# Performance work log

Hardware: AMD Instinct MI355X
Metric: run time of the kernel (lower is better)

## Reference

```python
import jax, jax.numpy as jnp
import numpy as np


def _sincos_1d(dim, L):
    # standard 1D sin-cos embedding: (L, dim), dim even
    half = dim // 2
    omega = 1.0 / (10000.0 ** (jnp.arange(half, dtype=jnp.float32) / half))  # (half,)
    out = jnp.arange(L, dtype=jnp.float32)[:, None] * omega[None, :]         # (L, half)
    return jnp.concatenate([jnp.sin(out), jnp.cos(out)], axis=1)            # (L, dim)


def setup_inputs() -> dict:
    key = jax.random.key(0)
    k1, k2, k3, k4 = jax.random.split(key, 4)
    B, C, T, H, W = 4, 2, 8, 128, 128
    D, P = 512, 32
    y_obs = jax.random.normal(k1, (B, C, T, H, W), dtype=jnp.float32)
    mask1 = jax.random.randint(k2, (B, 1, T, H, W), 0, 2).astype(jnp.int32)
    y_obs = y_obs * mask1.astype(jnp.float32)  # unobserved voxels are 0
    proj_w = jax.random.normal(k3, (D, C + 3 * P), dtype=jnp.float32) * 0.05
    proj_b = jax.random.normal(k4, (D,), dtype=jnp.float32) * 0.05
    return {"y_obs": y_obs, "mask1": mask1, "proj_w": proj_w, "proj_b": proj_b, "M_max": 65536}


def reference(y_obs, mask1, proj_w, proj_b, M_max):
    B, C, T, H, W = y_obs.shape
    N = T * H * W
    P = (proj_w.shape[1] - C) // 3  # pos_dim_each
    et = _sincos_1d(P, T)  # (T, P)
    eh = _sincos_1d(P, H)  # (H, P)
    ew = _sincos_1d(P, W)  # (W, P)

    # stream-compact nonzero voxel positions (row-major order = torch nonzero order)
    mflat = (mask1[:, 0].reshape(B, N) != 0)                       # (B, N)
    pos = jnp.where(mflat, jnp.arange(N, dtype=jnp.int32)[None, :], N)
    spos = jnp.sort(pos, axis=1)[:, :M_max]                        # (B, M)
    valid = spos < N                                               # (B, M)
    idx = jnp.minimum(spos, N - 1)                                 # safe gather index

    t_idx = idx // (H * W)
    h_idx = (idx // W) % H
    w_idx = idx % W

    # gather observed values: (B, M, C)
    vals = jnp.take_along_axis(y_obs.reshape(B, C, N), idx[:, None, :], axis=2)
    vals = jnp.transpose(vals, (0, 2, 1))

    feat = jnp.concatenate([vals, et[t_idx], eh[h_idx], ew[w_idx]], axis=-1)  # (B, M, C+3P)
    feat = jnp.where(valid[..., None], feat, 0.0)  # padded rows are zero features (torch pads zeros)

    cond_tokens = jnp.einsum('bmf,df->bmd', feat, proj_w) + proj_b  # (B, M, D)
    pad_mask = ~valid                                               # True == padding
    return cond_tokens, pad_mask
```

## Files before the change

### kernel.cpp

```cpp
#include <hip/hip_runtime.h>
#include <stdint.h>

#define BB    4
#define CC    2
#define TT    8
#define HH    128
#define WW    128
#define NN    131072
#define DD    512
#define PP    32
#define FF    98
#define KP    104
#define MMAX  65536

#define WT_OFF   0
#define CIDX_OFF 212992
#define TAB_OFF  (CIDX_OFF + 1048576)
#define CNT_OFF  (TAB_OFF + 33792)
#define OFFS_OFF (CNT_OFF + 8192)
#define TOT_OFF  (OFFS_OFF + 8192)

__global__ void k_prep(const float* __restrict__ w, float* __restrict__ tab,
                       float* __restrict__ wt) {
    int i = blockIdx.x * 256 + threadIdx.x;
    if (i < 8448) {
        int pos, j;
        if (i < 256)            { pos = i >> 5;            j = i & 31; }
        else if (i < 256+4096)  { int ii = i - 256;        pos = ii >> 5; j = ii & 31; }
        else                    { int ii = i - 256 - 4096; pos = ii >> 5; j = ii & 31; }
        int jj = (j < 16) ? j : (j - 16);
        float omega = 1.0f / powf(10000.0f, (float)jj * (1.0f/16.0f));
        float arg = (float)pos * omega;
        tab[i] = (j < 16) ? sinf(arg) : cosf(arg);
    }
    int k = i - 8448;
    if (k >= 0 && k < KP * DD) {
        int f = k >> 9, d = k & 511;
        wt[k] = (f < FF) ? w[d * FF + f] : 0.0f;
    }
}

__global__ void k_count(const int* __restrict__ mask, int* __restrict__ cnt) {
    int b = blockIdx.y;
    int i = blockIdx.x * 256 + threadIdx.x;
    int m = (mask[b * NN + i] != 0);
    uint64_t bal = __ballot(m);
    __shared__ int wc[4];
    int lane = threadIdx.x & 63, wv = threadIdx.x >> 6;
    if (lane == 0) wc[wv] = __popcll(bal);
    __syncthreads();
    if (threadIdx.x == 0) cnt[b * 512 + blockIdx.x] = wc[0] + wc[1] + wc[2] + wc[3];
}

__global__ void k_scan(const int* __restrict__ cnt, int* __restrict__ offs, int* __restrict__ tot) {
    int b = blockIdx.x, t = threadIdx.x;
    __shared__ int s[512];
    int v0 = cnt[b * 512 + t];
    s[t] = v0;
    __syncthreads();
    for (int off = 1; off < 512; off <<= 1) {
        int add = (t >= off) ? s[t - off] : 0;
        __syncthreads();
        s[t] += add;
        __syncthreads();
    }
    offs[b * 512 + t] = s[t] - v0;
    if (t == 511) tot[b] = s[511];
}

__global__ void k_scatter(const int* __restrict__ mask, const int* __restrict__ offs,
                          int* __restrict__ cidx) {
    int b = blockIdx.y;
    int i = blockIdx.x * 256 + threadIdx.x;
    int m = (mask[b * NN + i] != 0);
    uint64_t bal = __ballot(m);
    int lane = threadIdx.x & 63, wv = threadIdx.x >> 6;
    __shared__ int wc[4];
    if (lane == 0) wc[wv] = __popcll(bal);
    __syncthreads();
    int woff = 0;
    for (int k = 0; k < wv; ++k) woff += wc[k];
    int rank = __popcll(bal & ((1ull << lane) - 1ull));
    if (m) {
        int r = offs[b * 512 + blockIdx.x] + woff + rank;
        if (r < MMAX) cidx[b * MMAX + r] = i;
    }
}

__global__ __launch_bounds__(256) void k_gemm(
    const float* __restrict__ yobs, const int* __restrict__ cidx,
    const float* __restrict__ tab,  const float* __restrict__ wt,
    const float* __restrict__ bias, const int* __restrict__ tot,
    float* __restrict__ out, float* __restrict__ pm)
{
    __shared__ float As[KP][64];
    __shared__ float Bs[KP][64];
    int bid = blockIdx.x;
    int mt = bid & 1023;
    int b  = bid >> 10;
    int m0 = mt << 6;
    int tid = threadIdx.x;
    int totb = tot[b];

    if (tid < 64)
        pm[(b << 16) + m0 + tid] = ((m0 + tid) >= totb) ? 1.0f : 0.0f;

    {
        int m = tid & 63, q = tid >> 6;
        bool val = (m0 + m) < totb;
        int idx = 0, tt = 0, hh = 0, ww = 0;
        if (val) {
            idx = cidx[(b << 16) + m0 + m];
            tt = idx >> 14; hh = (idx >> 7) & 127; ww = idx & 127;
        }
        const float* et = tab;
        const float* eh = tab + 256;
        const float* ew = tab + 4352;
        for (int k = q; k < KP; k += 4) {
            float f = 0.0f;
            if (val) {
                if (k < 2)       f = yobs[((b * 2 + k) << 17) + idx];
                else if (k < 34) f = et[(tt << 5) + k - 2];
                else if (k < 66) f = eh[(hh << 5) + k - 34];
                else if (k < 98) f = ew[(ww << 5) + k - 66];
            }
            As[k][m] = f;
        }
    }

    int tx = tid & 15, ty = tid >> 4;
    const float4* ap = (const float4*)As + ty;
    const float4* bp = (const float4*)Bs + tx;

    for (int dt = 0; dt < 8; ++dt) {
        for (int i = tid; i < KP * 16; i += 256) {
            int f = i >> 4, d4 = i & 15;
            *(float4*)&Bs[f][d4 << 2] = *(const float4*)&wt[(f << 9) + (dt << 6) + (d4 << 2)];
        }
        __syncthreads();

        float acc[4][4] = {};
        #pragma unroll 4
        for (int k = 0; k < KP; ++k) {
            float4 a  = ap[k * 16];
            float4 w4 = bp[k * 16];
            float av[4] = {a.x, a.y, a.z, a.w};
            float wv[4] = {w4.x, w4.y, w4.z, w4.w};
            #pragma unroll
            for (int i = 0; i < 4; ++i)
                #pragma unroll
                for (int j = 0; j < 4; ++j)
                    acc[i][j] = fmaf(av[i], wv[j], acc[i][j]);
        }

        float4 b4 = *(const float4*)&bias[(dt << 6) + (tx << 2)];
        float bv[4] = {b4.x, b4.y, b4.z, b4.w};
        size_t row0 = ((size_t)((b << 16) + m0 + (ty << 2))) * DD + (dt << 6) + (tx << 2);
        #pragma unroll
        for (int i = 0; i < 4; ++i) {
            float4 r;
            r.x = acc[i][0] + bv[0];
            r.y = acc[i][1] + bv[1];
            r.z = acc[i][2] + bv[2];
            r.w = acc[i][3] + bv[3];
            *(float4*)&out[row0 + (size_t)i * DD] = r;
        }
        __syncthreads();
    }
}

extern "C" void kernel_launch(void* const* d_in, const int* in_sizes, int n_in,
                              void* d_out, int out_size, void* d_ws, size_t ws_size,
                              hipStream_t stream) {
    const float* yobs  = (const float*)d_in[0];
    const int*   mask  = (const int*)d_in[1];
    const float* projw = (const float*)d_in[2];
    const float* projb = (const float*)d_in[3];

    char* ws = (char*)d_ws;
    float* wt   = (float*)(ws + WT_OFF);
    int*   cidx = (int*)  (ws + CIDX_OFF);
    float* tab  = (float*)(ws + TAB_OFF);
    int*   cnt  = (int*)  (ws + CNT_OFF);
    int*   offs = (int*)  (ws + OFFS_OFF);
    int*   tot  = (int*)  (ws + TOT_OFF);

    float* cond = (float*)d_out;
    float* pm   = (float*)d_out + (size_t)BB * MMAX * DD;

    k_prep<<<(8448 + KP * DD + 255) / 256, 256, 0, stream>>>(projw, tab, wt);
    k_count<<<dim3(512, BB), 256, 0, stream>>>(mask, cnt);
    k_scan<<<BB, 512, 0, stream>>>(cnt, offs, tot);
    k_scatter<<<dim3(512, BB), 256, 0, stream>>>(mask, offs, cidx);
    k_gemm<<<BB * 1024, 256, 0, stream>>>(yobs, cidx, tab, wt, projb, tot, cond, pm);
}
```

Baseline: 797.2 us.

## Use split-bf16 MFMA for projection GEMM with swizzled LDS feature tile

Replaces the scalar fp32 FMA GEMM with bf16 MFMA 32x32x16 instructions. The fp32 accuracy is approximated by splitting each operand into high and low bf16 parts and summing three cross products. Weights are pre-split and laid out K-major in the prep kernel, with K padded to 128 and the channel values moved to the end. Features are gathered per row with float4 table loads into an XOR-swizzled LDS tile, and B fragments now come straight from global memory with no LDS staging. The aim is to cut ALU time so the kernel is limited by output bandwidth, at the cost of a slightly lower-precision result than true fp32.

```diff
diff --git a/kernel.cpp b/kernel.cpp
--- a/kernel.cpp
+++ b/kernel.cpp
@@ -3,25 +3,36 @@
 
 #define BB    4
 #define CC    2
-#define TT    8
-#define HH    128
-#define WW    128
 #define NN    131072
 #define DD    512
-#define PP    32
 #define FF    98
-#define KP    104
+#define K2    128
 #define MMAX  65536
 
-#define WT_OFF   0
-#define CIDX_OFF 212992
-#define TAB_OFF  (CIDX_OFF + 1048576)
-#define CNT_OFF  (TAB_OFF + 33792)
-#define OFFS_OFF (CNT_OFF + 8192)
-#define TOT_OFF  (OFFS_OFF + 8192)
+
+#define BTH_OFF  0
+#define BTL_OFF  131072
+#define TAB_OFF  262144
+#define CIDX_OFF 295936
+#define CNT_OFF  1344512
+#define OFFS_OFF 1352704
+#define TOT_OFF  1360896
+
+typedef short  s16x8  __attribute__((ext_vector_type(8)));
+typedef float  f32x16 __attribute__((ext_vector_type(16)));
+
+__device__ __forceinline__ unsigned short f2bf(float x) {
+    uint32_t u = __builtin_bit_cast(uint32_t, x);
+    u += 0x7fffu + ((u >> 16) & 1u);
+    return (unsigned short)(u >> 16);
+}
+__device__ __forceinline__ float bf2f(unsigned short h) {
+    uint32_t u = ((uint32_t)h) << 16;
+    return __builtin_bit_cast(float, u);
+}
 
 __global__ void k_prep(const float* __restrict__ w, float* __restrict__ tab,
-                       float* __restrict__ wt) {
+                       unsigned short* __restrict__ bth, unsigned short* __restrict__ btl) {
     int i = blockIdx.x * 256 + threadIdx.x;
     if (i < 8448) {
         int pos, j;
@@ -34,9 +45,14 @@
         tab[i] = (j < 16) ? sinf(arg) : cosf(arg);
     }
     int k = i - 8448;
-    if (k >= 0 && k < KP * DD) {
-        int f = k >> 9, d = k & 511;
-        wt[k] = (f < FF) ? w[d * FF + f] : 0.0f;
+    if (k >= 0 && k < DD * K2) {
+        int d = k >> 7, kk = k & 127;
+        float v = 0.0f;
+        if (kk < 96)      v = w[d * FF + kk + 2];
+        else if (kk < 98) v = w[d * FF + (kk - 96)];
+        unsigned short h = f2bf(v);
+        bth[k] = h;
+        btl[k] = f2bf(v - bf2f(h));
     }
 }
 
@@ -89,12 +105,12 @@
 
 __global__ __launch_bounds__(256) void k_gemm(
     const float* __restrict__ yobs, const int* __restrict__ cidx,
-    const float* __restrict__ tab,  const float* __restrict__ wt,
+    const float* __restrict__ tab,
+    const unsigned short* __restrict__ bth, const unsigned short* __restrict__ btl,
     const float* __restrict__ bias, const int* __restrict__ tot,
     float* __restrict__ out, float* __restrict__ pm)
 {
-    __shared__ float As[KP][64];
-    __shared__ float Bs[KP][64];
+    __shared__ unsigned short As[2][64 * 128];
     int bid = blockIdx.x;
     int mt = bid & 1023;
     int b  = bid >> 10;
@@ -106,66 +122,89 @@
         pm[(b << 16) + m0 + tid] = ((m0 + tid) >= totb) ? 1.0f : 0.0f;
 
     {
-        int m = tid & 63, q = tid >> 6;
-        bool val = (m0 + m) < totb;
-        int idx = 0, tt = 0, hh = 0, ww = 0;
+        int r = tid >> 2, s = tid & 3;
+        bool val = (m0 + r) < totb;
+        float v[32];
+        #pragma unroll
+        for (int j = 0; j < 32; ++j) v[j] = 0.0f;
         if (val) {
-            idx = cidx[(b << 16) + m0 + m];
-            tt = idx >> 14; hh = (idx >> 7) & 127; ww = idx & 127;
-        }
-        const float* et = tab;
-        const float* eh = tab + 256;
-        const float* ew = tab + 4352;
-        for (int k = q; k < KP; k += 4) {
-            float f = 0.0f;
-            if (val) {
-                if (k < 2)       f = yobs[((b * 2 + k) << 17) + idx];
-                else if (k < 34) f = et[(tt << 5) + k - 2];
-                else if (k < 66) f = eh[(hh << 5) + k - 34];
-                else if (k < 98) f = ew[(ww << 5) + k - 66];
+            int idx = cidx[(b << 16) + m0 + r];
+            if (s < 3) {
+                int p = (s == 0) ? (idx >> 14) : (s == 1) ? ((idx >> 7) & 127) : (idx & 127);
+                const float* base = tab + ((s == 0) ? 0 : (s == 1) ? 256 : 4352) + (p << 5);
+                const float4* b4 = (const float4*)base;
+                #pragma unroll
+                for (int q = 0; q < 8; ++q) {
+                    float4 f = b4[q];
+                    v[4*q] = f.x; v[4*q+1] = f.y; v[4*q+2] = f.z; v[4*q+3] = f.w;
+                }
+            } else {
+                v[0] = yobs[((size_t)(b * 2) << 17) + idx];
+                v[1] = yobs[((size_t)(b * 2 + 1) << 17) + idx];
             }
-            As[k][m] = f;
-        }
-    }
-
-    int tx = tid & 15, ty = tid >> 4;
-    const float4* ap = (const float4*)As + ty;
-    const float4* bp = (const float4*)Bs + tx;
+        }
+        uint32_t rowbase = (uint32_t)r * 256u;
+        uint32_t M = (uint32_t)(((r & 7) << 4) ^ (((r >> 3) & 1) << 7));
+        #pragma unroll
+        for (int c = 0; c < 4; ++c) {
+            uint32_t hp[4], lp[4];
+            #pragma unroll
+            for (int q = 0; q < 4; ++q) {
+                float a0 = v[c*8 + 2*q], a1 = v[c*8 + 2*q + 1];
+                unsigned short h0 = f2bf(a0), h1 = f2bf(a1);
+                unsigned short l0 = f2bf(a0 - bf2f(h0)), l1 = f2bf(a1 - bf2f(h1));
+                hp[q] = (uint32_t)h0 | ((uint32_t)h1 << 16);
+                lp[q] = (uint32_t)l0 | ((uint32_t)l1 << 16);
+            }
+            uint32_t byt = ((uint32_t)(s * 64 + c * 16)) ^ M;
+            *(uint4*)((char*)&As[0][0] + rowbase + byt) = make_uint4(hp[0], hp[1], hp[2], hp[3]);
+            *(uint4*)((char*)&As[1][0] + rowbase + byt) = make_uint4(lp[0], lp[1], lp[2], lp[3]);
+        }
+    }
+    __syncthreads();
+
+    int w = tid >> 6, l = tid & 63;
+    int wr = w >> 1, wc = w & 1;
+    int lrow = l & 31, lh = l >> 5;
+
+    int arow = wr * 32 + lrow;
+    uint32_t abase = (uint32_t)arow * 256u;
+    uint32_t AM = (uint32_t)(((arow & 7) << 4) ^ (((arow >> 3) & 1) << 7));
+    s16x8 afh[8], afl[8];
+    #pragma unroll
+    for (int ks = 0; ks < 8; ++ks) {
+        uint32_t byt = ((uint32_t)(ks * 32 + lh * 16)) ^ AM;
+        afh[ks] = *(const s16x8*)((char*)&As[0][0] + abase + byt);
+        afl[ks] = *(const s16x8*)((char*)&As[1][0] + abase + byt);
+    }
+
+    const unsigned short* bhp = bth + ((wc * 32 + lrow) << 7) + (lh << 3);
+    const unsigned short* blp = btl + ((wc * 32 + lrow) << 7) + (lh << 3);
 
     for (int dt = 0; dt < 8; ++dt) {
-        for (int i = tid; i < KP * 16; i += 256) {
-            int f = i >> 4, d4 = i & 15;
-            *(float4*)&Bs[f][d4 << 2] = *(const float4*)&wt[(f << 9) + (dt << 6) + (d4 << 2)];
-        }
-        __syncthreads();
-
-        float acc[4][4] = {};
-        #pragma unroll 4
-        for (int k = 0; k < KP; ++k) {
-            float4 a  = ap[k * 16];
-            float4 w4 = bp[k * 16];
-            float av[4] = {a.x, a.y, a.z, a.w};
-            float wv[4] = {w4.x, w4.y, w4.z, w4.w};
-            #pragma unroll
-            for (int i = 0; i < 4; ++i)
-                #pragma unroll
-                for (int j = 0; j < 4; ++j)
-                    acc[i][j] = fmaf(av[i], wv[j], acc[i][j]);
-        }
-
-        float4 b4 = *(const float4*)&bias[(dt << 6) + (tx << 2)];
-        float bv[4] = {b4.x, b4.y, b4.z, b4.w};
-        size_t row0 = ((size_t)((b << 16) + m0 + (ty << 2))) * DD + (dt << 6) + (tx << 2);
-        #pragma unroll
-        for (int i = 0; i < 4; ++i) {
-            float4 r;
-            r.x = acc[i][0] + bv[0];
-            r.y = acc[i][1] + bv[1];
-            r.z = acc[i][2] + bv[2];
-            r.w = acc[i][3] + bv[3];
-            *(float4*)&out[row0 + (size_t)i * DD] = r;
-        }
-        __syncthreads();
+        const unsigned short* bh = bhp + (dt << 13);
+        const unsigned short* bl = blp + (dt << 13);
+        s16x8 bfh[8], bfl[8];
+        #pragma unroll
+        for (int ks = 0; ks < 8; ++ks) {
+            bfh[ks] = *(const s16x8*)(bh + ks * 16);
+            bfl[ks] = *(const s16x8*)(bl + ks * 16);
+        }
+        f32x16 acc = {};
+        #pragma unroll
+        for (int ks = 0; ks < 8; ++ks) {
+            acc = __builtin_amdgcn_mfma_f32_32x32x16_bf16(afh[ks], bfh[ks], acc, 0, 0, 0);
+            acc = __builtin_amdgcn_mfma_f32_32x32x16_bf16(afh[ks], bfl[ks], acc, 0, 0, 0);
+            acc = __builtin_amdgcn_mfma_f32_32x32x16_bf16(afl[ks], bfh[ks], acc, 0, 0, 0);
+        }
+        int col = (dt << 6) + wc * 32 + lrow;
+        float bv = bias[col];
+        size_t obase = ((size_t)((b << 16) + m0 + wr * 32 + 4 * lh)) * DD + col;
+        #pragma unroll
+        for (int reg = 0; reg < 16; ++reg) {
+            int rrow = (reg & 3) + 8 * (reg >> 2);
+            out[obase + (size_t)rrow * DD] = acc[reg] + bv;
+        }
     }
 }
 
@@ -178,9 +217,10 @@
     const float* projb = (const float*)d_in[3];
 
     char* ws = (char*)d_ws;
-    float* wt   = (float*)(ws + WT_OFF);
+    unsigned short* bth = (unsigned short*)(ws + BTH_OFF);
+    unsigned short* btl = (unsigned short*)(ws + BTL_OFF);
+    float* tab  = (float*)(ws + TAB_OFF);
     int*   cidx = (int*)  (ws + CIDX_OFF);
-    float* tab  = (float*)(ws + TAB_OFF);
     int*   cnt  = (int*)  (ws + CNT_OFF);
     int*   offs = (int*)  (ws + OFFS_OFF);
     int*   tot  = (int*)  (ws + TOT_OFF);
@@ -188,9 +228,9 @@
     float* cond = (float*)d_out;
     float* pm   = (float*)d_out + (size_t)BB * MMAX * DD;
 
-    k_prep<<<(8448 + KP * DD + 255) / 256, 256, 0, stream>>>(projw, tab, wt);
+    k_prep<<<(8448 + DD * K2 + 255) / 256, 256, 0, stream>>>(projw, tab, bth, btl);
     k_count<<<dim3(512, BB), 256, 0, stream>>>(mask, cnt);
     k_scan<<<BB, 512, 0, stream>>>(cnt, offs, tot);
     k_scatter<<<dim3(512, BB), 256, 0, stream>>>(mask, offs, cidx);
-    k_gemm<<<BB * 1024, 256, 0, stream>>>(yobs, cidx, tab, wt, projb, tot, cond, pm);
-}
+    k_gemm<<<BB * 1024, 256, 0, stream>>>(yobs, cidx, tab, bth, btl, projb, tot, cond, pm);
+}
```

Measured after the change: 720.8 us. -9.6%, faster.
